# Kernel tuning notes

Measured on AMD Instinct MI355X. Metric: run time of the kernel, lower is better.

Reference implementation:

```python
import jax, jax.numpy as jnp
import numpy as np

B, T, E, H, R = 4, 256, 128, 8, 64
D = E // H


def _xavier(k, fan_in, fan_out, gain=1.0):
    a = gain * np.sqrt(6.0 / (fan_in + fan_out))
    return jax.random.uniform(k, (fan_in, fan_out), minval=-a, maxval=a, dtype=jnp.float32)


def setup_inputs() -> dict:
    key = jax.random.key(0)
    ks = jax.random.split(key, 16)
    g = 1.0 / np.sqrt(2.0)  # gain used for q/k/v when qkv_same_dim
    return {
        "query": jax.random.normal(ks[0], (B, T, E), jnp.float32),
        "velocity": jax.random.normal(ks[1], (B, T, 3, E), jnp.float32),
        "edge_feature": jax.random.normal(ks[2], (B, T, T, R), jnp.float32),
        "edge_direction": jax.random.normal(ks[3], (B, T, T, 3), jnp.float32),
        "cutoff": jax.random.uniform(ks[4], (B, T, T), jnp.float32),
        "Wq": _xavier(ks[5], E, E, g), "bq": jnp.zeros((E,), jnp.float32),
        "Wk": _xavier(ks[6], E, E, g), "bk": jnp.zeros((E,), jnp.float32),
        "Wv": _xavier(ks[7], E, 3 * E, g), "bv": jnp.zeros((3 * E,), jnp.float32),
        "Wo": _xavier(ks[8], E, 3 * E), "bo": jnp.zeros((3 * E,), jnp.float32),
        "Wvel": _xavier(ks[9], E, 3 * E), "bvel": jnp.zeros((3 * E,), jnp.float32),
        "Wdk": _xavier(ks[10], R, E), "bdk": jnp.zeros((E,), jnp.float32),
        "Wdv": _xavier(ks[11], R, 3 * E), "bdv": jnp.zeros((3 * E,), jnp.float32),
    }


def reference(query, velocity, edge_feature, edge_direction, cutoff,
              Wq, bq, Wk, bk, Wv, bv, Wo, bo, Wvel, bvel, Wdk, bdk, Wdv, bdv):
    b, t, e = query.shape
    h = H
    d = e // h
    scaling = d ** -0.5
    # projections
    q = ((query @ Wq + bq) * scaling).reshape(b, t, 1, h, d)   # [b,t,1,h,d]
    k = (query @ Wk + bk).reshape(b, 1, t, h, d)                # [b,1,t,h,d]
    v = (query @ Wv + bv).reshape(b, 1, t, h, 3 * d)            # [b,1,t,h,3d]
    # RBF distance gates (dense pairwise)
    dk = jax.nn.silu(edge_feature @ Wdk + bdk).reshape(b, t, t, h, d)
    dv = jax.nn.silu(edge_feature @ Wdv + bdv).reshape(b, t, t, h, 3 * d)
    v = v * dv                                                  # [b,t,t,h,3d]
    v, vp1, vp2 = jnp.split(v, 3, axis=-1)                      # each [b,t,t,h,d]
    # velocity channel
    velp = velocity @ Wvel + bvel                               # [b,t,3,3e]
    w1, w2, w3 = jnp.split(velp, 3, axis=-1)                    # each [b,t,3,e]
    velocity_dot = (w1 * w2).sum(axis=2)                        # [b,t,e]
    vel_r = velocity.reshape(b, t, 3, h, d)
    # elementwise (non-dot-product) attention weights
    aw = q * k * dk / np.float32(np.sqrt(d))                    # [b,t,t,h,d]
    awf = jnp.nan_to_num(jax.nn.softmax(aw, axis=2))
    c = cutoff[..., None, None]                                 # [b,t,t,1,1]
    attn = (awf * c * v * (c != 0)).sum(axis=2).reshape(b, t, e)
    o1, o2, o3 = jnp.split(attn @ Wo + bo, 3, axis=-1)          # each [b,t,e]
    # equivariant vector path
    vec1 = vel_r[:, None] * vp1[:, :, :, None]                  # [b,t,t,3,h,d]
    vec2 = vp2[:, :, :, None] * edge_direction[..., None, None]
    vec = ((vec1 + vec2).reshape(b, t, t, 3, e) * (c != 0)).sum(axis=2)  # [b,t,3,e]
    dx = velocity_dot * o2 + o3                                 # [b,t,e]
    dvec = w3 * o1[:, :, None, :] + vec                         # [b,t,3,e]
    return dx, dvec
```

## Files before the change

### kernel.cpp

```cpp
#include <hip/hip_runtime.h>
#include <hip/hip_bf16.h>
#include <math.h>

#define TT 256
#define EE 128
#define TJ 16
#define SRCB 28672
#define TSH 14336

typedef __attribute__((ext_vector_type(8))) short short8v;
typedef __attribute__((ext_vector_type(4))) short short4v;
typedef __attribute__((ext_vector_type(4))) float f32x4;

__device__ __forceinline__ float silu_f(float x) {
    return x * __builtin_amdgcn_rcpf(1.0f + __expf(-x));
}

__device__ __forceinline__ unsigned short f2bf(float f) {
    union { float f; unsigned u; } x; x.f = f;
    unsigned r = (x.u + 0x7FFFu + ((x.u >> 16) & 1u)) >> 16;
    return (unsigned short)r;
}

__device__ __forceinline__ unsigned cvt_pk_bf16(float lo, float hi) {
    unsigned r;
    asm("v_cvt_pk_bf16_f32 %0, %1, %2" : "=v"(r) : "v"(lo), "v"(hi));
    return r;
}

__device__ __forceinline__ float bflo(unsigned u) { return __uint_as_float(u << 16); }
__device__ __forceinline__ float bfhi(unsigned u) { return __uint_as_float(u & 0xffff0000u); }
__device__ __forceinline__ float bfu(unsigned short u) { return __uint_as_float(((unsigned)u) << 16); }

__global__ __launch_bounds__(256) void packW_kernel(
    const float* __restrict__ Wdk, const float* __restrict__ Wdv,
    unsigned short* __restrict__ wfrag) {
    const int idx = blockIdx.x * 256 + threadIdx.x;
    const int lane = idx & 63;
    const int kh = (idx >> 6) & 1;
    const int nn = (idx >> 7) & 7;
    const int w = idx >> 10;
    const float* Wsel; int wstride, colbase;
    if (w == 0) { Wsel = Wdk; wstride = 128; colbase = 0; }
    else { Wsel = Wdv; wstride = 384; colbase = (w - 1) * 128; }
    const int lrow = lane >> 4;
    const int lcol = lane & 15;
    const int col = colbase + nn * 16 + lcol;
    unsigned short* dst = wfrag + (size_t)idx * 8;
#pragma unroll
    for (int e = 0; e < 8; ++e) {
        const int k = kh * 32 + lrow * 8 + e;
        dst[e] = f2bf(Wsel[k * wstride + col]);
    }
}

__global__ __launch_bounds__(256) void phaseA_kernel(
    const float* __restrict__ query, const float* __restrict__ velocity,
    const float* __restrict__ Wq, const float* __restrict__ bq,
    const float* __restrict__ Wk, const float* __restrict__ bk,
    const float* __restrict__ Wv, const float* __restrict__ bv,
    const float* __restrict__ Wvel, const float* __restrict__ bvel,
    float* __restrict__ qs_ws, unsigned short* __restrict__ kkvvT,
    float* __restrict__ veldot_ws, float* __restrict__ w3_ws) {
    const int row = blockIdx.x;
    const int t = threadIdx.x;
    __shared__ float sIn[EE];
    __shared__ float sVel[3 * EE];
    __shared__ float sVelp[3 * 384];
    if (t < EE) sIn[t] = query[(size_t)row * EE + t];
    for (int idx = t; idx < 3 * EE; idx += 256)
        sVel[idx] = velocity[(size_t)row * 3 * EE + idx];
    __syncthreads();

    unsigned short* tb = kkvvT + (size_t)(row >> 4) * TSH;
    const int r16 = row & 15;
    for (int o = t; o < 640; o += 256) {
        if (o < 128) {
            int c = o;
            float acc = bq[c];
#pragma unroll 8
            for (int r = 0; r < 128; ++r) acc = fmaf(sIn[r], Wq[r * 128 + c], acc);
            qs_ws[(size_t)row * 128 + c] = acc * 0.25f;
        } else if (o < 256) {
            int c = o - 128;
            float acc = bk[c];
#pragma unroll 8
            for (int r = 0; r < 128; ++r) acc = fmaf(sIn[r], Wk[r * 128 + c], acc);
            const int sg = (r16 >> 2) ^ ((c >> 2) & 3);
            tb[c * 16 + sg * 4 + (r16 & 3)] = f2bf(acc);
        } else {
            int c = o - 256;
            float acc = bv[c];
#pragma unroll 8
            for (int r = 0; r < 128; ++r) acc = fmaf(sIn[r], Wv[r * 384 + c], acc);
            const int col = 128 + c;
            const int sg = (r16 >> 2) ^ ((col >> 2) & 3);
            tb[col * 16 + sg * 4 + (r16 & 3)] = f2bf(acc);
        }
    }
    for (int idx = t; idx < 384; idx += 256)
        tb[8192 + r16 * 384 + idx] = f2bf(sVel[idx]);

    for (int c = t; c < 384; c += 256) {
        float a0 = bvel[c], a1 = a0, a2 = a0;
#pragma unroll 8
        for (int r = 0; r < 128; ++r) {
            float w = Wvel[r * 384 + c];
            a0 = fmaf(sVel[r], w, a0);
            a1 = fmaf(sVel[128 + r], w, a1);
            a2 = fmaf(sVel[256 + r], w, a2);
        }
        sVelp[0 * 384 + c] = a0;
        sVelp[1 * 384 + c] = a1;
        sVelp[2 * 384 + c] = a2;
    }
    __syncthreads();
    if (t < 128) {
        int c = t;
        float vd = 0.f;
#pragma unroll
        for (int s = 0; s < 3; ++s)
            vd += sVelp[s * 384 + c] * sVelp[s * 384 + 128 + c];
        veldot_ws[(size_t)row * 128 + c] = vd;
#pragma unroll
        for (int s = 0; s < 3; ++s)
            w3_ws[((size_t)row * 3 + s) * 128 + c] = sVelp[s * 384 + 256 + c];
    }
}

__global__ __launch_bounds__(256, 3) void phaseB_kernel(
    const float* __restrict__ edge_feature, const float* __restrict__ edge_direction,
    const float* __restrict__ cutoff,
    const unsigned short* __restrict__ wfrag, const unsigned short* __restrict__ kkvvT,
    const float* __restrict__ bdk, const float* __restrict__ bdv,
    const float* __restrict__ qs_ws,
    float* __restrict__ attn_ws, float* __restrict__ vec_ws) {
    const int blk = blockIdx.x;
    const int x = blk & 7;
    const int slot = blk >> 3;
    const int b = x >> 1;
    const int i = ((x & 1) << 7) + slot;
    const int row = b * TT + i;

    const int t = threadIdx.x;
    const int wave = t >> 6;
    const int lane = t & 63;
    const int lrow = lane >> 4;
    const int lcol = lane & 15;

    __shared__ __align__(16) unsigned char sSrc[SRCB];
    __shared__ __align__(16) unsigned char sEFb[16 * 128];
    __shared__ unsigned short sKD[128 * 18];
    __shared__ unsigned short sGV[3 * 128 * 18];
    __shared__ float sCut[TJ];
    __shared__ float sDirS[TJ * 3];
    __shared__ float sMrg[128][5];

    const float* Bsel;
    int colbase;
    if (wave == 0) { Bsel = bdk; colbase = 0; }
    else { Bsel = bdv; colbase = (wave - 1) * 128; }

    float biasv[8];
#pragma unroll
    for (int n = 0; n < 8; ++n)
        biasv[n] = Bsel[colbase + n * 16 + lcol];

    const unsigned short* wfbase = wfrag + ((size_t)wave * 1024 + lane) * 8;
    short8v bwr[16];
#pragma unroll
    for (int n = 0; n < 8; ++n) {
        bwr[2 * n]     = *(const short8v*)(wfbase + (size_t)n * 1024);
        bwr[2 * n + 1] = *(const short8v*)(wfbase + (size_t)n * 1024 + 512);
    }

    const int grp = t >> 7;
    const int c = t & 127;
    const float qsc = qs_ws[(size_t)row * 128 + c] * 0.25f;

    float l = 0.f, A = 0.f;
    float v0 = 0.f, v1 = 0.f, v2 = 0.f;

    const size_t ef_base = (size_t)row * TT * 64;
    const size_t cut_base = (size_t)row * TT;
    const size_t dir_base = (size_t)row * TT * 3;
    const unsigned char* kvT = (const unsigned char*)kkvvT + (size_t)(b * 16) * SRCB;

    const int ldsoff = (t & 192) * 16;
    const int gswz = (lrow ^ ((lcol >> 2) & 3)) * 4;

#pragma unroll
    for (int r = 0; r < 7; ++r)
        __builtin_amdgcn_global_load_lds(
            (const void*)(kvT + (size_t)r * 4096 + (size_t)t * 16),
            (void*)(sSrc + r * 4096 + ldsoff), 16, 0, 0);

    f32x4 pEf = ((const f32x4*)(edge_feature + ef_base))[t];
    float pCut = (t < TJ) ? cutoff[cut_base + t] : 0.f;
    float pDir = (t < TJ * 3) ? edge_direction[dir_base + t] : 0.f;

    for (int j0 = 0; j0 < TT; j0 += TJ) {
        {
            const int erow = t >> 4;
            const int kq = t & 15;
            unsigned plo = cvt_pk_bf16(pEf[0], pEf[1]);
            unsigned phi = cvt_pk_bf16(pEf[2], pEf[3]);
            const int byteoff = (kq * 8) ^ ((erow & 7) << 4);
            *(int2*)(sEFb + erow * 128 + byteoff) = make_int2((int)plo, (int)phi);
            if (t < TJ) sCut[t] = pCut;
            if (t < TJ * 3) sDirS[t] = pDir;
        }
        __syncthreads();

        {
            const int jn = (j0 + TJ) & 255;
            pEf = ((const f32x4*)(edge_feature + ef_base + (size_t)jn * 64))[t];
            pCut = (t < TJ) ? cutoff[cut_base + jn + t] : 0.f;
            pDir = (t < TJ * 3) ? edge_direction[dir_base + (size_t)jn * 3 + t] : 0.f;
        }

        {
            const unsigned short* gT = (const unsigned short*)sSrc;
            const int arow = lcol;
            const int swzb = (arow & 7) << 4;
            const short8v a0 = *(const short8v*)(sEFb + arow * 128 + ((lrow * 16) ^ swzb));
            const short8v a1 = *(const short8v*)(sEFb + arow * 128 + ((64 + lrow * 16) ^ swzb));

            short4v g4[8];
#pragma unroll
            for (int n = 0; n < 8; ++n)
                g4[n] = *(const short4v*)(gT + ((wave * 128 + n * 16 + lcol) * 16 + gswz));
#pragma unroll
            for (int n = 0; n < 8; ++n) {
                const int col = colbase + n * 16 + lcol;
                f32x4 acc = {biasv[n], biasv[n], biasv[n], biasv[n]};
                acc = __builtin_amdgcn_mfma_f32_16x16x32_bf16(a0, bwr[2 * n],     acc, 0, 0, 0);
                acc = __builtin_amdgcn_mfma_f32_16x16x32_bf16(a1, bwr[2 * n + 1], acc, 0, 0, 0);
                const float r0 = bfu((unsigned short)g4[n][0]) * silu_f(acc[0]);
                const float r1 = bfu((unsigned short)g4[n][1]) * silu_f(acc[1]);
                const float r2 = bfu((unsigned short)g4[n][2]) * silu_f(acc[2]);
                const float r3 = bfu((unsigned short)g4[n][3]) * silu_f(acc[3]);
                const unsigned w01 = cvt_pk_bf16(r0, r1);
                const unsigned w23 = cvt_pk_bf16(r2, r3);
                unsigned short* dst;
                if (wave == 0) {
                    dst = &sKD[col * 18 + lrow * 4];
                } else {
                    const int plane = (col >> 4) % 3;
                    const int cch = (col / 48) * 16 + lcol;
                    dst = &sGV[plane * 2304 + cch * 18 + lrow * 4];
                }
                *(unsigned*)(dst) = w01;
                *(unsigned*)(dst + 2) = w23;
            }
        }
        __syncthreads();

        if (j0 + TJ < TT) {
            const unsigned char* src = kvT + (size_t)((j0 >> 4) + 1) * SRCB;
#pragma unroll
            for (int r = 0; r < 4; ++r)
                __builtin_amdgcn_global_load_lds(
                    (const void*)(src + (size_t)r * 4096 + (size_t)t * 16),
                    (void*)(sSrc + r * 4096 + ldsoff), 16, 0, 0);
        }

        {
            const unsigned short* svel = (const unsigned short*)(sSrc + 16384);
            const int jlo = grp * (TJ / 2);
#pragma unroll
            for (int q = 0; q < 4; ++q) {
                const int jj = jlo + 2 * q;
                const unsigned kd2 = *(const unsigned*)(&sKD[c * 18 + jj]);
                const unsigned vg2 = *(const unsigned*)(&sGV[0 * 2304 + c * 18 + jj]);
                const unsigned p12 = *(const unsigned*)(&sGV[1 * 2304 + c * 18 + jj]);
                const unsigned p22 = *(const unsigned*)(&sGV[2 * 2304 + c * 18 + jj]);
                const float cut0 = sCut[jj];
                const float cut1 = sCut[jj + 1];
                const float p0 = __expf(qsc * bflo(kd2));
                const float p1 = __expf(qsc * bfhi(kd2));
                l += p0 + p1;
                A = fmaf(p0 * cut0, bflo(vg2), A);
                A = fmaf(p1 * cut1, bfhi(vg2), A);
                if (cut0 != 0.0f) {
                    const unsigned short* vp = svel + (size_t)jj * 384 + c;
                    const float w1 = bflo(p12), w2 = bflo(p22);
                    v0 = fmaf(bfu(vp[0]),   w1, fmaf(w2, sDirS[jj * 3 + 0], v0));
                    v1 = fmaf(bfu(vp[128]), w1, fmaf(w2, sDirS[jj * 3 + 1], v1));
                    v2 = fmaf(bfu(vp[256]), w1, fmaf(w2, sDirS[jj * 3 + 2], v2));
                }
                if (cut1 != 0.0f) {
                    const unsigned short* vp = svel + (size_t)(jj + 1) * 384 + c;
                    const float w1 = bfhi(p12), w2 = bfhi(p22);
                    v0 = fmaf(bfu(vp[0]),   w1, fmaf(w2, sDirS[jj * 3 + 3], v0));
                    v1 = fmaf(bfu(vp[128]), w1, fmaf(w2, sDirS[jj * 3 + 4], v1));
                    v2 = fmaf(bfu(vp[256]), w1, fmaf(w2, sDirS[jj * 3 + 5], v2));
                }
            }
        }
        __syncthreads();

        if (j0 + TJ < TT) {
            const unsigned char* src = kvT + (size_t)((j0 >> 4) + 1) * SRCB;
#pragma unroll
            for (int r = 4; r < 7; ++r)
                __builtin_amdgcn_global_load_lds(
                    (const void*)(src + (size_t)r * 4096 + (size_t)t * 16),
                    (void*)(sSrc + r * 4096 + ldsoff), 16, 0, 0);
        }
    }

    if (grp == 1) {
        sMrg[c][0] = l;  sMrg[c][1] = A;
        sMrg[c][2] = v0; sMrg[c][3] = v1; sMrg[c][4] = v2;
    }
    __syncthreads();
    if (grp == 0) {
        const float L = l + sMrg[c][0];
        const float Aa = A + sMrg[c][1];
        const float attn = (L > 0.f) ? (Aa * __builtin_amdgcn_rcpf(L)) : 0.f;
        attn_ws[(size_t)row * 128 + c] = attn;
        vec_ws[((size_t)row * 3 + 0) * 128 + c] = v0 + sMrg[c][2];
        vec_ws[((size_t)row * 3 + 1) * 128 + c] = v1 + sMrg[c][3];
        vec_ws[((size_t)row * 3 + 2) * 128 + c] = v2 + sMrg[c][4];
    }
}

__global__ __launch_bounds__(256) void phaseC_kernel(
    const float* __restrict__ Wo, const float* __restrict__ bo,
    const float* __restrict__ attn_ws, const float* __restrict__ veldot_ws,
    const float* __restrict__ w3_ws, const float* __restrict__ vec_ws,
    float* __restrict__ out) {
    const int row = blockIdx.x;
    const int t = threadIdx.x;
    __shared__ float sAttn[128];
    __shared__ float sO[384];
    if (t < 128) sAttn[t] = attn_ws[(size_t)row * 128 + t];
    __syncthreads();
    for (int o = t; o < 384; o += 256) {
        float acc = bo[o];
#pragma unroll 8
        for (int r = 0; r < 128; ++r) acc = fmaf(sAttn[r], Wo[r * 384 + o], acc);
        sO[o] = acc;
    }
    __syncthreads();
    if (t < 128) {
        int c = t;
        float o1 = sO[c], o2 = sO[128 + c], o3 = sO[256 + c];
        float dx = fmaf(veldot_ws[(size_t)row * 128 + c], o2, o3);
        out[(size_t)row * 128 + c] = dx;
#pragma unroll
        for (int s = 0; s < 3; ++s) {
            size_t idx = ((size_t)row * 3 + s) * 128 + c;
            out[131072 + idx] = fmaf(w3_ws[idx], o1, vec_ws[idx]);
        }
    }
}

extern "C" void kernel_launch(void* const* d_in, const int* in_sizes, int n_in,
                              void* d_out, int out_size, void* d_ws, size_t ws_size,
                              hipStream_t stream) {
    (void)in_sizes; (void)n_in; (void)out_size; (void)ws_size;
    const float* query          = (const float*)d_in[0];
    const float* velocity       = (const float*)d_in[1];
    const float* edge_feature   = (const float*)d_in[2];
    const float* edge_direction = (const float*)d_in[3];
    const float* cutoff         = (const float*)d_in[4];
    const float* Wq   = (const float*)d_in[5];  const float* bq   = (const float*)d_in[6];
    const float* Wk   = (const float*)d_in[7];  const float* bk   = (const float*)d_in[8];
    const float* Wv   = (const float*)d_in[9];  const float* bv   = (const float*)d_in[10];
    const float* Wo   = (const float*)d_in[11]; const float* bo   = (const float*)d_in[12];
    const float* Wvel = (const float*)d_in[13]; const float* bvel = (const float*)d_in[14];
    const float* Wdk  = (const float*)d_in[15]; const float* bdk  = (const float*)d_in[16];
    const float* Wdv  = (const float*)d_in[17]; const float* bdv  = (const float*)d_in[18];

    float* ws        = (float*)d_ws;
    float* qs_ws     = ws;
    float* veldot_ws = ws + 131072;
    float* w3_ws     = ws + 262144;
    float* attn_ws   = ws + 655360;
    float* vec_ws    = ws + 786432;
    unsigned short* wfrag = (unsigned short*)(ws + 1179648);
    unsigned short* kkvvT = (unsigned short*)(ws + 1196032);

    float* out = (float*)d_out;

    hipLaunchKernelGGL(packW_kernel, dim3(16), dim3(256), 0, stream,
        Wdk, Wdv, wfrag);
    hipLaunchKernelGGL(phaseA_kernel, dim3(1024), dim3(256), 0, stream,
        query, velocity, Wq, bq, Wk, bk, Wv, bv, Wvel, bvel,
        qs_ws, kkvvT, veldot_ws, w3_ws);
    hipLaunchKernelGGL(phaseB_kernel, dim3(1024), dim3(256), 0, stream,
        edge_feature, edge_direction, cutoff,
        wfrag, kkvvT, bdk, bdv, qs_ws, attn_ws, vec_ws);
    hipLaunchKernelGGL(phaseC_kernel, dim3(1024), dim3(256), 0, stream,
        Wo, bo, attn_ws, veldot_ws, w3_ws, vec_ws, out);
}
```

Baseline: 150.4 us.

## Double-buffer velocity and edge-feature tiles to drop one barrier per step

Splits the shared staging buffer into a gates region and a double-buffered velocity region. Edge features, cutoff and direction are also double-buffered, with the next tile written during the accumulation phase. This removes one __syncthreads per j-tile and issues the velocity prefetch earlier so it overlaps with the MFMA stage. It also folds log2(e) into the query scale so exp2f can replace __expf, and lowers the launch-bounds occupancy hint from 3 to 2 because the larger LDS footprint reduces blocks per CU.

```diff
diff --git a/kernel.cpp b/kernel.cpp
--- a/kernel.cpp
+++ b/kernel.cpp
@@ -7,6 +7,8 @@
 #define TJ 16
 #define SRCB 28672
 #define TSH 14336
+#define GTB 16384
+#define VTB 12288
 
 typedef __attribute__((ext_vector_type(8))) short short8v;
 typedef __attribute__((ext_vector_type(4))) short short4v;
@@ -128,7 +130,7 @@
     }
 }
 
-__global__ __launch_bounds__(256, 3) void phaseB_kernel(
+__global__ __launch_bounds__(256, 2) void phaseB_kernel(
     const float* __restrict__ edge_feature, const float* __restrict__ edge_direction,
     const float* __restrict__ cutoff,
     const unsigned short* __restrict__ wfrag, const unsigned short* __restrict__ kkvvT,
@@ -148,12 +150,13 @@
     const int lrow = lane >> 4;
     const int lcol = lane & 15;
 
-    __shared__ __align__(16) unsigned char sSrc[SRCB];
-    __shared__ __align__(16) unsigned char sEFb[16 * 128];
+    __shared__ __align__(16) unsigned char sGates[GTB];
+    __shared__ __align__(16) unsigned char sVelB[2 * VTB];
+    __shared__ __align__(16) unsigned char sEFb[2 * 2048];
     __shared__ unsigned short sKD[128 * 18];
     __shared__ unsigned short sGV[3 * 128 * 18];
-    __shared__ float sCut[TJ];
-    __shared__ float sDirS[TJ * 3];
+    __shared__ float sCut[2][TJ];
+    __shared__ float sDirS[2][TJ * 3];
     __shared__ float sMrg[128][5];
 
     const float* Bsel;
@@ -176,7 +179,7 @@
 
     const int grp = t >> 7;
     const int c = t & 127;
-    const float qsc = qs_ws[(size_t)row * 128 + c] * 0.25f;
+    const float qsc = qs_ws[(size_t)row * 128 + c] * 0.25f * 1.44269504f;
 
     float l = 0.f, A = 0.f;
     float v0 = 0.f, v1 = 0.f, v2 = 0.f;
@@ -190,41 +193,55 @@
     const int gswz = (lrow ^ ((lcol >> 2) & 3)) * 4;
 
 #pragma unroll
-    for (int r = 0; r < 7; ++r)
+    for (int r = 0; r < 4; ++r)
         __builtin_amdgcn_global_load_lds(
             (const void*)(kvT + (size_t)r * 4096 + (size_t)t * 16),
-            (void*)(sSrc + r * 4096 + ldsoff), 16, 0, 0);
-
-    f32x4 pEf = ((const f32x4*)(edge_feature + ef_base))[t];
-    float pCut = (t < TJ) ? cutoff[cut_base + t] : 0.f;
-    float pDir = (t < TJ * 3) ? edge_direction[dir_base + t] : 0.f;
-
+            (void*)(sGates + r * 4096 + ldsoff), 16, 0, 0);
+#pragma unroll
+    for (int r = 0; r < 3; ++r)
+        __builtin_amdgcn_global_load_lds(
+            (const void*)(kvT + GTB + (size_t)r * 4096 + (size_t)t * 16),
+            (void*)(sVelB + r * 4096 + ldsoff), 16, 0, 0);
+
+    {
+        f32x4 e0 = ((const f32x4*)(edge_feature + ef_base))[t];
+        const int erow = t >> 4;
+        const int kq = t & 15;
+        const unsigned plo = cvt_pk_bf16(e0[0], e0[1]);
+        const unsigned phi = cvt_pk_bf16(e0[2], e0[3]);
+        const int byteoff = (kq * 8) ^ ((erow & 7) << 4);
+        *(int2*)(sEFb + erow * 128 + byteoff) = make_int2((int)plo, (int)phi);
+        if (t < TJ) sCut[0][t] = cutoff[cut_base + t];
+        if (t < TJ * 3) sDirS[0][t] = edge_direction[dir_base + t];
+    }
+    __syncthreads();
+
+    f32x4 pEf;
+    float pCut = 0.f, pDir = 0.f;
+    int e = 0;
     for (int j0 = 0; j0 < TT; j0 += TJ) {
-        {
-            const int erow = t >> 4;
-            const int kq = t & 15;
-            unsigned plo = cvt_pk_bf16(pEf[0], pEf[1]);
-            unsigned phi = cvt_pk_bf16(pEf[2], pEf[3]);
-            const int byteoff = (kq * 8) ^ ((erow & 7) << 4);
-            *(int2*)(sEFb + erow * 128 + byteoff) = make_int2((int)plo, (int)phi);
-            if (t < TJ) sCut[t] = pCut;
-            if (t < TJ * 3) sDirS[t] = pDir;
-        }
-        __syncthreads();
-
+        if (j0 + TJ < TT) {
+            const unsigned char* src = kvT + (size_t)((j0 >> 4) + 1) * SRCB + GTB;
+            unsigned char* dst = sVelB + (e ^ 1) * VTB;
+#pragma unroll
+            for (int r = 0; r < 3; ++r)
+                __builtin_amdgcn_global_load_lds(
+                    (const void*)(src + (size_t)r * 4096 + (size_t)t * 16),
+                    (void*)(dst + r * 4096 + ldsoff), 16, 0, 0);
+        }
         {
             const int jn = (j0 + TJ) & 255;
             pEf = ((const f32x4*)(edge_feature + ef_base + (size_t)jn * 64))[t];
             pCut = (t < TJ) ? cutoff[cut_base + jn + t] : 0.f;
             pDir = (t < TJ * 3) ? edge_direction[dir_base + (size_t)jn * 3 + t] : 0.f;
         }
-
         {
-            const unsigned short* gT = (const unsigned short*)sSrc;
+            const unsigned short* gT = (const unsigned short*)sGates;
+            const unsigned char* efb = sEFb + e * 2048;
             const int arow = lcol;
             const int swzb = (arow & 7) << 4;
-            const short8v a0 = *(const short8v*)(sEFb + arow * 128 + ((lrow * 16) ^ swzb));
-            const short8v a1 = *(const short8v*)(sEFb + arow * 128 + ((64 + lrow * 16) ^ swzb));
+            const short8v a0 = *(const short8v*)(efb + arow * 128 + ((lrow * 16) ^ swzb));
+            const short8v a1 = *(const short8v*)(efb + arow * 128 + ((64 + lrow * 16) ^ swzb));
 
             short4v g4[8];
 #pragma unroll
@@ -262,11 +279,23 @@
             for (int r = 0; r < 4; ++r)
                 __builtin_amdgcn_global_load_lds(
                     (const void*)(src + (size_t)r * 4096 + (size_t)t * 16),
-                    (void*)(sSrc + r * 4096 + ldsoff), 16, 0, 0);
-        }
-
+                    (void*)(sGates + r * 4096 + ldsoff), 16, 0, 0);
+        }
         {
-            const unsigned short* svel = (const unsigned short*)(sSrc + 16384);
+            unsigned char* efb = sEFb + (e ^ 1) * 2048;
+            const int erow = t >> 4;
+            const int kq = t & 15;
+            const unsigned plo = cvt_pk_bf16(pEf[0], pEf[1]);
+            const unsigned phi = cvt_pk_bf16(pEf[2], pEf[3]);
+            const int byteoff = (kq * 8) ^ ((erow & 7) << 4);
+            *(int2*)(efb + erow * 128 + byteoff) = make_int2((int)plo, (int)phi);
+            if (t < TJ) sCut[e ^ 1][t] = pCut;
+            if (t < TJ * 3) sDirS[e ^ 1][t] = pDir;
+        }
+        {
+            const unsigned short* svel = (const unsigned short*)(sVelB + e * VTB);
+            const float* cutE = sCut[e];
+            const float* dirE = sDirS[e];
             const int jlo = grp * (TJ / 2);
 #pragma unroll
             for (int q = 0; q < 4; ++q) {
@@ -275,39 +304,31 @@
                 const unsigned vg2 = *(const unsigned*)(&sGV[0 * 2304 + c * 18 + jj]);
                 const unsigned p12 = *(const unsigned*)(&sGV[1 * 2304 + c * 18 + jj]);
                 const unsigned p22 = *(const unsigned*)(&sGV[2 * 2304 + c * 18 + jj]);
-                const float cut0 = sCut[jj];
-                const float cut1 = sCut[jj + 1];
-                const float p0 = __expf(qsc * bflo(kd2));
-                const float p1 = __expf(qsc * bfhi(kd2));
+                const float cut0 = cutE[jj];
+                const float cut1 = cutE[jj + 1];
+                const float p0 = exp2f(qsc * bflo(kd2));
+                const float p1 = exp2f(qsc * bfhi(kd2));
                 l += p0 + p1;
                 A = fmaf(p0 * cut0, bflo(vg2), A);
                 A = fmaf(p1 * cut1, bfhi(vg2), A);
                 if (cut0 != 0.0f) {
                     const unsigned short* vp = svel + (size_t)jj * 384 + c;
                     const float w1 = bflo(p12), w2 = bflo(p22);
-                    v0 = fmaf(bfu(vp[0]),   w1, fmaf(w2, sDirS[jj * 3 + 0], v0));
-                    v1 = fmaf(bfu(vp[128]), w1, fmaf(w2, sDirS[jj * 3 + 1], v1));
-                    v2 = fmaf(bfu(vp[256]), w1, fmaf(w2, sDirS[jj * 3 + 2], v2));
+                    v0 = fmaf(bfu(vp[0]),   w1, fmaf(w2, dirE[jj * 3 + 0], v0));
+                    v1 = fmaf(bfu(vp[128]), w1, fmaf(w2, dirE[jj * 3 + 1], v1));
+                    v2 = fmaf(bfu(vp[256]), w1, fmaf(w2, dirE[jj * 3 + 2], v2));
                 }
                 if (cut1 != 0.0f) {
                     const unsigned short* vp = svel + (size_t)(jj + 1) * 384 + c;
                     const float w1 = bfhi(p12), w2 = bfhi(p22);
-                    v0 = fmaf(bfu(vp[0]),   w1, fmaf(w2, sDirS[jj * 3 + 3], v0));
-                    v1 = fmaf(bfu(vp[128]), w1, fmaf(w2, sDirS[jj * 3 + 4], v1));
-                    v2 = fmaf(bfu(vp[256]), w1, fmaf(w2, sDirS[jj * 3 + 5], v2));
+                    v0 = fmaf(bfu(vp[0]),   w1, fmaf(w2, dirE[jj * 3 + 3], v0));
+                    v1 = fmaf(bfu(vp[128]), w1, fmaf(w2, dirE[jj * 3 + 4], v1));
+                    v2 = fmaf(bfu(vp[256]), w1, fmaf(w2, dirE[jj * 3 + 5], v2));
                 }
             }
         }
         __syncthreads();
-
-        if (j0 + TJ < TT) {
-            const unsigned char* src = kvT + (size_t)((j0 >> 4) + 1) * SRCB;
-#pragma unroll
-            for (int r = 4; r < 7; ++r)
-                __builtin_amdgcn_global_load_lds(
-                    (const void*)(src + (size_t)r * 4096 + (size_t)t * 16),
-                    (void*)(sSrc + r * 4096 + ldsoff), 16, 0, 0);
-        }
+        e ^= 1;
     }
 
     if (grp == 1) {
```

Result: no change. 152.8 us (+1.6%).
